# Optimization experiments

Hardware: AMD Instinct MI355X
Metric: run time of the kernel (lower is better)

## Reference

```python
import jax, jax.numpy as jnp
import numpy as np
import math

B, S, D, H = 2, 2048, 1024, 16
DH = D // H  # dim_per_head = 64


def setup_inputs() -> dict:
    key = jax.random.key(0)
    ks = jax.random.split(key, 12)
    s = 1.0 / math.sqrt(D)
    return {
        "key": jax.random.normal(ks[0], (B, S, D), jnp.float32),
        "value": jax.random.normal(ks[1], (B, S, D), jnp.float32),
        "query": jax.random.normal(ks[2], (B, S, D), jnp.float32),
        "mask": jax.random.randint(ks[3], (B, S, S), 0, 2).astype(bool),
        "Wq": jax.random.normal(ks[4], (D, D), jnp.float32) * s,
        "bq": jnp.zeros((D,), jnp.float32),
        "Wk": jax.random.normal(ks[5], (D, D), jnp.float32) * s,
        "bk": jnp.zeros((D,), jnp.float32),
        "Wv": jax.random.normal(ks[6], (D, D), jnp.float32) * s,
        "bv": jnp.zeros((D,), jnp.float32),
        "Wo": jax.random.normal(ks[7], (D, D), jnp.float32) * s,
        "bo": jnp.zeros((D,), jnp.float32),
    }


def _shape(x):
    # [B, S, D] -> [B, H, S, DH]
    return x.reshape(B, -1, H, DH).transpose(0, 2, 1, 3)


def reference(key, value, query, mask, Wq, bq, Wk, bk, Wv, bv, Wo, bo):
    q = _shape(query @ Wq.T + bq)  # [B,H,Sq,DH]
    k = _shape(key @ Wk.T + bk)    # [B,H,Sk,DH]
    v = _shape(value @ Wv.T + bv)  # [B,H,Sk,DH]
    q = q / jnp.sqrt(jnp.asarray(DH, q.dtype))
    scores = jnp.einsum("bhqd,bhkd->bhqk", q, k)
    scores = jnp.where(mask[:, None, :, :], jnp.asarray(-1e18, scores.dtype), scores)
    attn = jax.nn.softmax(scores, axis=-1)
    # dropout is identity in eval/deterministic reference
    ctx = jnp.einsum("bhqk,bhkd->bhqd", attn, v)
    ctx = ctx.transpose(0, 2, 1, 3).reshape(B, -1, D)  # unshape
    return ctx @ Wo.T + bo
```

## Files before the change

### kernel.cpp

```cpp
#include <hip/hip_runtime.h>
#include <math.h>


constexpr int Bc  = 2;
constexpr int Sc  = 2048;
constexpr int Dc  = 1024;
constexpr int Hc  = 16;
constexpr int DHc = 64;
constexpr int BSc = Bc * Sc;

constexpr float LOG2E = 1.4426950408889634f;

typedef __bf16 bf16x8 __attribute__((ext_vector_type(8)));
typedef __bf16 bf16x4 __attribute__((ext_vector_type(4)));
typedef float  f32x4  __attribute__((ext_vector_type(4)));

#define GLDS16(gp, lp) __builtin_amdgcn_global_load_lds( \
    (const __attribute__((address_space(1))) void*)(gp), \
    (__attribute__((address_space(3))) void*)(lp), 16, 0, 0)

__global__ __launch_bounds__(256)
void wsplit(const float* __restrict__ W0, const float* __restrict__ W1,
            const float* __restrict__ W2, const float* __restrict__ W3,
            __bf16* __restrict__ out)
{
    const float* src[4] = {W0, W1, W2, W3};
    const int z = blockIdx.y;
    const size_t idx = ((size_t)blockIdx.x * 256 + threadIdx.x) * 4;
    const float4 v = *(const float4*)&src[z][idx];
    bf16x4 o;
    o[0] = (__bf16)v.x; o[1] = (__bf16)v.y; o[2] = (__bf16)v.z; o[3] = (__bf16)v.w;
    *(bf16x4*)&out[(size_t)z * Dc * Dc + idx] = o;
}

__device__ __forceinline__ void sweep128s(const float* __restrict__ A,
                                          const __bf16* __restrict__ Wh,
                                          __bf16* As, __bf16* Ws,
                                          int gm0, int gn0, f32x4 acc[4][4])
{
    const int tid  = threadIdx.x;
    const int w    = tid >> 6;
    const int lane = tid & 63;
    const int cc   = lane & 15;
    const int g    = lane >> 4;
    const int wm   = (w & 1) * 64;
    const int wn   = (w >> 1) * 64;

    for (int k0 = 0; k0 < Dc; k0 += 64) {
        __syncthreads();
#pragma unroll
        for (int r = 0; r < 4; ++r) {
            const int L  = r * 256 + tid;
            const int wr = L >> 3;
            const int sl = L & 7;
            const int c  = sl ^ (wr & 7);
            GLDS16(Wh + (size_t)(gn0 + wr) * Dc + k0 + c * 8,
                   (char*)Ws + (r * 256 + w * 64) * 16);
        }
#pragma unroll
        for (int i = 0; i < 8; ++i) {
            const int Lq = i * 256 + tid;
            const int ar = Lq >> 4;
            const int aq = Lq & 15;
            const float4 v = *(const float4*)&A[(size_t)(gm0 + ar) * Dc + k0 + aq * 4];
            const int off = ar * 128 +
                        ((((aq >> 1) ^ (ar & 7)) << 4) | ((aq & 1) << 3));
            bf16x4 hv;
            hv[0] = (__bf16)v.x; hv[1] = (__bf16)v.y;
            hv[2] = (__bf16)v.z; hv[3] = (__bf16)v.w;
            *(bf16x4*)((char*)As + off) = hv;
        }
        __syncthreads();
#pragma unroll
        for (int kk = 0; kk < 2; ++kk) {
            const int cb4 = (kk * 4 + g) << 4;
            bf16x8 af[4], bfr[4];
#pragma unroll
            for (int mt = 0; mt < 4; ++mt) {
                const int row = wm + mt * 16 + cc;
                af[mt] = *(const bf16x8*)((const char*)As + row * 128 +
                                          (cb4 ^ ((row & 7) << 4)));
            }
#pragma unroll
            for (int nt = 0; nt < 4; ++nt) {
                const int row = wn + nt * 16 + cc;
                bfr[nt] = *(const bf16x8*)((const char*)Ws + row * 128 +
                                           (cb4 ^ ((row & 7) << 4)));
            }
#pragma unroll
            for (int mt = 0; mt < 4; ++mt)
#pragma unroll
                for (int nt = 0; nt < 4; ++nt)
                    acc[mt][nt] = __builtin_amdgcn_mfma_f32_16x16x32_bf16(
                        af[mt], bfr[nt], acc[mt][nt], 0, 0, 0);
        }
    }
}

__device__ __forceinline__ void sweep64b(const __bf16* __restrict__ Ahi,
                                         const __bf16* __restrict__ Alo,
                                         const __bf16* __restrict__ Wh,
                                         __bf16* AsHi, __bf16* AsLo, __bf16* Ws,
                                         int gm0, int gn0, f32x4 acc[2][4])
{
    const int tid  = threadIdx.x;
    const int w    = tid >> 6;
    const int lane = tid & 63;
    const int cc   = lane & 15;
    const int g    = lane >> 4;
    const int wm   = (w & 1) * 32;
    const int wn   = (w >> 1) * 64;

    for (int k0 = 0; k0 < Dc; k0 += 64) {
        __syncthreads();
#pragma unroll
        for (int r = 0; r < 4; ++r) {
            const int L  = r * 256 + tid;
            const int wr = L >> 3;
            const int sl = L & 7;
            const int c  = sl ^ (wr & 7);
            GLDS16(Wh + (size_t)(gn0 + wr) * Dc + k0 + c * 8,
                   (char*)Ws + (r * 256 + w * 64) * 16);
        }
#pragma unroll
        for (int r = 0; r < 2; ++r) {
            const int L  = r * 256 + tid;
            const int wr = L >> 3;
            const int sl = L & 7;
            const int c  = sl ^ (wr & 7);
            GLDS16(Ahi + (size_t)(gm0 + wr) * Dc + k0 + c * 8,
                   (char*)AsHi + (r * 256 + w * 64) * 16);
            GLDS16(Alo + (size_t)(gm0 + wr) * Dc + k0 + c * 8,
                   (char*)AsLo + (r * 256 + w * 64) * 16);
        }
        __syncthreads();
#pragma unroll
        for (int kk = 0; kk < 2; ++kk) {
            const int cb4 = (kk * 4 + g) << 4;
            bf16x8 ahi[2], alo[2], bfr[4];
#pragma unroll
            for (int mt = 0; mt < 2; ++mt) {
                const int row = wm + mt * 16 + cc;
                const int off = row * 128 + (cb4 ^ ((row & 7) << 4));
                ahi[mt] = *(const bf16x8*)((const char*)AsHi + off);
                alo[mt] = *(const bf16x8*)((const char*)AsLo + off);
            }
#pragma unroll
            for (int nt = 0; nt < 4; ++nt) {
                const int row = wn + nt * 16 + cc;
                bfr[nt] = *(const bf16x8*)((const char*)Ws + row * 128 +
                                           (cb4 ^ ((row & 7) << 4)));
            }
#pragma unroll
            for (int mt = 0; mt < 2; ++mt)
#pragma unroll
                for (int nt = 0; nt < 4; ++nt) {
                    acc[mt][nt] = __builtin_amdgcn_mfma_f32_16x16x32_bf16(
                        ahi[mt], bfr[nt], acc[mt][nt], 0, 0, 0);
                    acc[mt][nt] = __builtin_amdgcn_mfma_f32_16x16x32_bf16(
                        alo[mt], bfr[nt], acc[mt][nt], 0, 0, 0);
                }
        }
    }
}

__global__ __launch_bounds__(256)
void qkv_mfma(const float* __restrict__ query, const float* __restrict__ key,
              const float* __restrict__ value, const __bf16* __restrict__ Whi,
              const float* __restrict__ bq, const float* __restrict__ bk,
              const float* __restrict__ bv,
              __bf16* __restrict__ Qo, __bf16* __restrict__ Ko, __bf16* __restrict__ Vt)
{
    __shared__ __align__(16) __bf16 As[8192];
    __shared__ __align__(16) __bf16 Ws[8192];

    const int z = blockIdx.z;
    const float* A    = (z == 0) ? query : (z == 1) ? key : value;
    const float* bias = (z == 0) ? bq    : (z == 1) ? bk  : bv;
    const float scale = (z == 0) ? 0.125f * LOG2E : 1.0f;
    const __bf16* Wh  = Whi + (size_t)z * Dc * Dc;

    const int gm0 = blockIdx.x * 128;
    const int gn0 = blockIdx.y * 128;

    f32x4 acc[4][4];
#pragma unroll
    for (int mt = 0; mt < 4; ++mt)
#pragma unroll
        for (int nt = 0; nt < 4; ++nt) acc[mt][nt] = {0.f, 0.f, 0.f, 0.f};

    sweep128s(A, Wh, As, Ws, gm0, gn0, acc);

    const int tid = threadIdx.x;
    const int w = tid >> 6, lane = tid & 63;
    const int cc = lane & 15, g = lane >> 4;
    const int wm = (w & 1) * 64, wn = (w >> 1) * 64;

    float bias4[4];
#pragma unroll
    for (int nt = 0; nt < 4; ++nt) bias4[nt] = bias[gn0 + wn + nt * 16 + cc];

    if (z == 2) {
#pragma unroll
        for (int mt = 0; mt < 4; ++mt)
#pragma unroll
            for (int nt = 0; nt < 4; ++nt) {
                const int col = gn0 + wn + nt * 16 + cc;
                const int h = col >> 6, dh = col & 63;
                const int row0 = gm0 + wm + mt * 16 + g * 4;
                const int b = row0 >> 11, s0 = row0 & 2047;
                bf16x4 vv;
#pragma unroll
                for (int reg = 0; reg < 4; ++reg)
                    vv[reg] = (__bf16)(acc[mt][nt][reg] + bias4[nt]);
                *(bf16x4*)&Vt[(((size_t)(b * Hc + h)) * DHc + dh) * Sc + s0] = vv;
            }
    } else {
        __bf16* O = (z == 0) ? Qo : Ko;
#pragma unroll
        for (int mt = 0; mt < 4; ++mt)
#pragma unroll
            for (int nt = 0; nt < 4; ++nt) {
                const int col = gn0 + wn + nt * 16 + cc;
                const int h = col >> 6, dh = col & 63;
#pragma unroll
                for (int reg = 0; reg < 4; ++reg) {
                    const int row = gm0 + wm + mt * 16 + g * 4 + reg;
                    const int b = row >> 11, s = row & 2047;
                    O[(((size_t)(b * Hc + h)) * Sc + s) * DHc + dh] =
                        (__bf16)((acc[mt][nt][reg] + bias4[nt]) * scale);
                }
            }
    }
}

__global__ __launch_bounds__(256)
void out_mfma(const __bf16* __restrict__ ctxHi, const __bf16* __restrict__ ctxLo,
              const __bf16* __restrict__ Wohi,
              const float* __restrict__ bo, float* __restrict__ out)
{
    __shared__ __align__(16) __bf16 AsHi[4096];
    __shared__ __align__(16) __bf16 AsLo[4096];
    __shared__ __align__(16) __bf16 Ws[8192];

    const int gm0 = blockIdx.x * 64;
    const int gn0 = blockIdx.y * 128;

    f32x4 acc[2][4];
#pragma unroll
    for (int mt = 0; mt < 2; ++mt)
#pragma unroll
        for (int nt = 0; nt < 4; ++nt) acc[mt][nt] = {0.f, 0.f, 0.f, 0.f};

    sweep64b(ctxHi, ctxLo, Wohi, AsHi, AsLo, Ws, gm0, gn0, acc);

    const int tid = threadIdx.x;
    const int w = tid >> 6, lane = tid & 63;
    const int cc = lane & 15, g = lane >> 4;
    const int wm = (w & 1) * 32, wn = (w >> 1) * 64;

    float bias4[4];
#pragma unroll
    for (int nt = 0; nt < 4; ++nt) bias4[nt] = bo[gn0 + wn + nt * 16 + cc];

#pragma unroll
    for (int mt = 0; mt < 2; ++mt)
#pragma unroll
        for (int nt = 0; nt < 4; ++nt) {
            const int col = gn0 + wn + nt * 16 + cc;
#pragma unroll
            for (int reg = 0; reg < 4; ++reg) {
                const int row = gm0 + wm + mt * 16 + g * 4 + reg;
                out[(size_t)row * Dc + col] = acc[mt][nt][reg] + bias4[nt];
            }
        }
}

__global__ __launch_bounds__(256)
void mask_pack(const int* __restrict__ mask, unsigned long long* __restrict__ out)
{
    const int lane = threadIdx.x & 63;
    const size_t waveBase = ((size_t)blockIdx.x * 4 + (threadIdx.x >> 6)) * 256;
    unsigned long long b0 = __ballot(mask[waveBase + lane]        != 0);
    unsigned long long b1 = __ballot(mask[waveBase + 64 + lane]   != 0);
    unsigned long long b2 = __ballot(mask[waveBase + 128 + lane]  != 0);
    unsigned long long b3 = __ballot(mask[waveBase + 192 + lane]  != 0);
    if (lane == 0) {
        unsigned long long* dst = out + (waveBase >> 6);
        dst[0] = b0; dst[1] = b1; dst[2] = b2; dst[3] = b3;
    }
}

__global__ __launch_bounds__(512, 6)
void attn_mfma(const __bf16* __restrict__ Q, const __bf16* __restrict__ K,
               const __bf16* __restrict__ Vt,
               const unsigned long long* __restrict__ mp,
               __bf16* __restrict__ ctxHi, __bf16* __restrict__ ctxLo)
{
    __shared__ __align__(16) char smem[53248];

    const int tid  = threadIdx.x;
    const int w    = tid >> 6;
    const int lane = tid & 63;
    const int cc   = lane & 15;
    const int g    = lane >> 4;
    const int qg   = w & 3;
    const int kh   = w >> 2;
    const int bh   = blockIdx.y;
    const int b    = bh >> 4;
    const int h    = bh & 15;
    const int qw   = blockIdx.x * 64 + qg * 16;

    const __bf16* Qb  = Q  + (size_t)bh * Sc * DHc;
    const __bf16* Kb  = K  + (size_t)bh * Sc * DHc;
    const __bf16* Vtb = Vt + (size_t)bh * DHc * Sc;

    __bf16* Ks = (__bf16*)(smem + kh * 18432);
    __bf16* Vs = (__bf16*)(smem + kh * 18432 + 9216);
    char*   Pw = smem + 36864 + w * 2048;

    const bf16x8 qa0 = *(const bf16x8*)&Qb[(size_t)(qw + cc) * DHc + g * 8];
    const bf16x8 qa1 = *(const bf16x8*)&Qb[(size_t)(qw + cc) * DHc + 32 + g * 8];

    f32x4 o[4] = {};
    float l[4] = {0.f, 0.f, 0.f, 0.f};

    const int t4    = tid & 255;
    const int str_r = t4 >> 3;
    const int str_c = (t4 & 7) * 8;
    const int kbase = kh * (Sc / 2);

    bf16x8 pk0 = *(const bf16x8*)&Kb[(size_t)(kbase + str_r) * DHc + str_c];
    bf16x8 pk1 = *(const bf16x8*)&Kb[(size_t)(kbase + str_r + 32) * DHc + str_c];
    bf16x8 pv0 = *(const bf16x8*)&Vtb[(size_t)str_r * Sc + kbase + str_c];
    bf16x8 pv1 = *(const bf16x8*)&Vtb[(size_t)(str_r + 32) * Sc + kbase + str_c];

    for (int it = 0; it < 16; ++it) {
        const int k0 = kbase + it * 64;
        __syncthreads();
        *(bf16x8*)&Ks[(size_t)str_r * 72 + str_c]        = pk0;
        *(bf16x8*)&Ks[(size_t)(str_r + 32) * 72 + str_c] = pk1;
        *(bf16x8*)&Vs[(size_t)str_r * 72 + str_c]        = pv0;
        *(bf16x8*)&Vs[(size_t)(str_r + 32) * 72 + str_c] = pv1;
        __syncthreads();

        if (it < 15) {
            const int kn = k0 + 64;
            pk0 = *(const bf16x8*)&Kb[(size_t)(kn + str_r) * DHc + str_c];
            pk1 = *(const bf16x8*)&Kb[(size_t)(kn + str_r + 32) * DHc + str_c];
            pv0 = *(const bf16x8*)&Vtb[(size_t)str_r * Sc + kn + str_c];
            pv1 = *(const bf16x8*)&Vtb[(size_t)(str_r + 32) * Sc + kn + str_c];
        }

        unsigned long long mw[4];
#pragma unroll
        for (int r = 0; r < 4; ++r)
            mw[r] = mp[(size_t)(b * Sc + qw + g * 4 + r) * (Sc / 64) + (k0 >> 6)];

        f32x4 sc[4];
#pragma unroll
        for (int nt = 0; nt < 4; ++nt) {
            const bf16x8 kb0 = *(const bf16x8*)&Ks[(size_t)(nt * 16 + cc) * 72 + g * 8];
            const bf16x8 kb1 = *(const bf16x8*)&Ks[(size_t)(nt * 16 + cc) * 72 + 32 + g * 8];
            f32x4 z = {-24.f, -24.f, -24.f, -24.f};
            z = __builtin_amdgcn_mfma_f32_16x16x32_bf16(qa0, kb0, z, 0, 0, 0);
            z = __builtin_amdgcn_mfma_f32_16x16x32_bf16(qa1, kb1, z, 0, 0, 0);
            sc[nt] = z;
        }

        unsigned mlo[4], mhi[4];
#pragma unroll
        for (int r = 0; r < 4; ++r) {
            const unsigned long long sh = mw[r] >> cc;
            mlo[r] = (unsigned)sh;
            mhi[r] = (unsigned)(sh >> 32);
        }
#pragma unroll
        for (int nt = 0; nt < 4; ++nt)
#pragma unroll
            for (int r = 0; r < 4; ++r) {
                float p = __builtin_amdgcn_exp2f(sc[nt][r]);
                const unsigned bit =
                    (nt == 0) ? (mlo[r] & 1u) :
                    (nt == 1) ? (mlo[r] & 0x10000u) :
                    (nt == 2) ? (mhi[r] & 1u) : (mhi[r] & 0x10000u);
                p = bit ? 0.f : p;
                l[r] += p;
                *(__bf16*)(Pw + (g * 4 + r) * 128 + (((nt ^ g) << 5) | (cc << 1))) =
                    (__bf16)p;
            }

        const int sw = (cc >> 2) << 5;
        const bf16x8 pa0 = *(const bf16x8*)(Pw + cc * 128 + ((g * 16) ^ sw));
        const bf16x8 pa1 = *(const bf16x8*)(Pw + cc * 128 + ((64 + g * 16) ^ sw));

#pragma unroll
        for (int nt = 0; nt < 4; ++nt) {
            const bf16x8 vb0 = *(const bf16x8*)&Vs[(size_t)(nt * 16 + cc) * 72 + g * 8];
            const bf16x8 vb1 = *(const bf16x8*)&Vs[(size_t)(nt * 16 + cc) * 72 + 32 + g * 8];
            o[nt] = __builtin_amdgcn_mfma_f32_16x16x32_bf16(pa0, vb0, o[nt], 0, 0, 0);
            o[nt] = __builtin_amdgcn_mfma_f32_16x16x32_bf16(pa1, vb1, o[nt], 0, 0, 0);
        }
    }

#pragma unroll
    for (int off = 1; off < 16; off <<= 1)
#pragma unroll
        for (int r = 0; r < 4; ++r)
            l[r] += __shfl_xor(l[r], off, 16);

    __syncthreads();
    float* Oc = (float*)smem;
    float* Lc = (float*)(smem + 16384);
    if (kh) {
#pragma unroll
        for (int nt = 0; nt < 4; ++nt)
#pragma unroll
            for (int r = 0; r < 4; ++r)
                Oc[(qg * 16 + g * 4 + r) * 64 + nt * 16 + cc] = o[nt][r];
        if (cc == 0)
#pragma unroll
            for (int r = 0; r < 4; ++r) Lc[qg * 16 + g * 4 + r] = l[r];
    }
    __syncthreads();
    if (!kh) {
#pragma unroll
        for (int r = 0; r < 4; ++r) {
            const float lt = l[r] + Lc[qg * 16 + g * 4 + r];
            const float inv = 1.0f / lt;
            const int q = qw + g * 4 + r;
#pragma unroll
            for (int nt = 0; nt < 4; ++nt) {
                const size_t idx = ((size_t)b * Sc + q) * Dc + h * 64 + nt * 16 + cc;
                const float v =
                    (o[nt][r] + Oc[(qg * 16 + g * 4 + r) * 64 + nt * 16 + cc]) * inv;
                const __bf16 hi = (__bf16)v;
                ctxHi[idx] = hi;
                ctxLo[idx] = (__bf16)(v - (float)hi);
            }
        }
    }
}

extern "C" void kernel_launch(void* const* d_in, const int* in_sizes, int n_in,
                              void* d_out, int out_size, void* d_ws, size_t ws_size,
                              hipStream_t stream)
{
    const float* key   = (const float*)d_in[0];
    const float* value = (const float*)d_in[1];
    const float* query = (const float*)d_in[2];
    const int*   mask  = (const int*)  d_in[3];
    const float* Wq    = (const float*)d_in[4];
    const float* bq    = (const float*)d_in[5];
    const float* Wk    = (const float*)d_in[6];
    const float* bk    = (const float*)d_in[7];
    const float* Wv    = (const float*)d_in[8];
    const float* bv    = (const float*)d_in[9];
    const float* Wo    = (const float*)d_in[10];
    const float* bo    = (const float*)d_in[11];
    float* out = (float*)d_out;

    char* wsb = (char*)d_ws;
    __bf16* Qbf  = (__bf16*)(wsb);
    __bf16* Kbf  = (__bf16*)(wsb + ((size_t)8  << 20));
    __bf16* Vt   = (__bf16*)(wsb + ((size_t)16 << 20));
    unsigned long long* mpk = (unsigned long long*)(wsb + ((size_t)32 << 20));
    __bf16* Whi  = (__bf16*)(wsb + ((size_t)33 << 20));
    __bf16* ctxHi = (__bf16*)(wsb + ((size_t)41 << 20));
    __bf16* ctxLo = (__bf16*)(wsb + ((size_t)49 << 20));

    dim3 gws(Dc * Dc / (256 * 4), 4);
    wsplit<<<gws, 256, 0, stream>>>(Wq, Wk, Wv, Wo, Whi);

    dim3 gqkv(BSc / 128, Dc / 128, 3);
    qkv_mfma<<<gqkv, 256, 0, stream>>>(query, key, value, Whi, bq, bk, bv,
                                       Qbf, Kbf, Vt);

    const int mask_n = Bc * Sc * Sc;
    mask_pack<<<mask_n / 1024, 256, 0, stream>>>(mask, mpk);

    dim3 gattn(Sc / 64, Bc * Hc);
    attn_mfma<<<gattn, 512, 0, stream>>>(Qbf, Kbf, Vt, mpk, ctxHi, ctxLo);

    dim3 gout(BSc / 64, Dc / 128);
    out_mfma<<<gout, 256, 0, stream>>>(ctxHi, ctxLo, Whi + (size_t)3 * Dc * Dc,
                                       bo, out);
}
```

Baseline: 300.1 us.

## Double query rows per attention wave and XOR-swizzle K/V shared tiles

Each attention block now covers 128 queries instead of 64, with every wave handling two 16-row query tiles. This reuses each K/V fragment loaded from shared memory for twice the MFMA work and halves the number of K/V tile loads across the grid. The padded 72-element LDS rows are replaced by unpadded 128-byte rows with an XOR swizzle to avoid bank conflicts while saving shared memory. In exchange, register pressure rises (occupancy hint lowered from 6 to 4) and the grid has half as many blocks.

```diff
diff --git a/kernel.cpp b/kernel.cpp
--- a/kernel.cpp
+++ b/kernel.cpp
@@ -291,13 +291,13 @@
     }
 }
 
-__global__ __launch_bounds__(512, 6)
+__global__ __launch_bounds__(512, 4)
 void attn_mfma(const __bf16* __restrict__ Q, const __bf16* __restrict__ K,
                const __bf16* __restrict__ Vt,
                const unsigned long long* __restrict__ mp,
                __bf16* __restrict__ ctxHi, __bf16* __restrict__ ctxLo)
 {
-    __shared__ __align__(16) char smem[53248];
+    __shared__ __align__(16) char smem[49152];
 
     const int tid  = threadIdx.x;
     const int w    = tid >> 6;
@@ -309,136 +309,167 @@
     const int bh   = blockIdx.y;
     const int b    = bh >> 4;
     const int h    = bh & 15;
-    const int qw   = blockIdx.x * 64 + qg * 16;
+    const int qw   = blockIdx.x * 128 + qg * 32;
 
     const __bf16* Qb  = Q  + (size_t)bh * Sc * DHc;
     const __bf16* Kb  = K  + (size_t)bh * Sc * DHc;
     const __bf16* Vtb = Vt + (size_t)bh * DHc * Sc;
 
-    __bf16* Ks = (__bf16*)(smem + kh * 18432);
-    __bf16* Vs = (__bf16*)(smem + kh * 18432 + 9216);
-    char*   Pw = smem + 36864 + w * 2048;
-
-    const bf16x8 qa0 = *(const bf16x8*)&Qb[(size_t)(qw + cc) * DHc + g * 8];
-    const bf16x8 qa1 = *(const bf16x8*)&Qb[(size_t)(qw + cc) * DHc + 32 + g * 8];
-
-    f32x4 o[4] = {};
-    float l[4] = {0.f, 0.f, 0.f, 0.f};
-
-    const int t4    = tid & 255;
-    const int str_r = t4 >> 3;
-    const int str_c = (t4 & 7) * 8;
+    char* Ks = smem + kh * 16384;
+    char* Vs = smem + kh * 16384 + 8192;
+    char* Pw = smem + 32768 + w * 2048;
+
+    bf16x8 qa[2][2];
+#pragma unroll
+    for (int mt = 0; mt < 2; ++mt) {
+        qa[mt][0] = *(const bf16x8*)&Qb[(size_t)(qw + mt * 16 + cc) * DHc + g * 8];
+        qa[mt][1] = *(const bf16x8*)&Qb[(size_t)(qw + mt * 16 + cc) * DHc + 32 + g * 8];
+    }
+
+    f32x4 o[2][4] = {};
+    float l[2][4] = {};
+
+    const int t4 = tid & 255;
+    const int sr = t4 >> 3;
+    const int sl = t4 & 7;
+    const int ck = sl ^ (sr & 7);
     const int kbase = kh * (Sc / 2);
 
-    bf16x8 pk0 = *(const bf16x8*)&Kb[(size_t)(kbase + str_r) * DHc + str_c];
-    bf16x8 pk1 = *(const bf16x8*)&Kb[(size_t)(kbase + str_r + 32) * DHc + str_c];
-    bf16x8 pv0 = *(const bf16x8*)&Vtb[(size_t)str_r * Sc + kbase + str_c];
-    bf16x8 pv1 = *(const bf16x8*)&Vtb[(size_t)(str_r + 32) * Sc + kbase + str_c];
+    bf16x8 pk0 = *(const bf16x8*)&Kb[(size_t)(kbase + sr) * DHc + ck * 8];
+    bf16x8 pk1 = *(const bf16x8*)&Kb[(size_t)(kbase + sr + 32) * DHc + ck * 8];
+    bf16x8 pv0 = *(const bf16x8*)&Vtb[(size_t)sr * Sc + kbase + ck * 8];
+    bf16x8 pv1 = *(const bf16x8*)&Vtb[(size_t)(sr + 32) * Sc + kbase + ck * 8];
 
     for (int it = 0; it < 16; ++it) {
         const int k0 = kbase + it * 64;
         __syncthreads();
-        *(bf16x8*)&Ks[(size_t)str_r * 72 + str_c]        = pk0;
-        *(bf16x8*)&Ks[(size_t)(str_r + 32) * 72 + str_c] = pk1;
-        *(bf16x8*)&Vs[(size_t)str_r * 72 + str_c]        = pv0;
-        *(bf16x8*)&Vs[(size_t)(str_r + 32) * 72 + str_c] = pv1;
+        *(bf16x8*)(Ks + sr * 128 + sl * 16)        = pk0;
+        *(bf16x8*)(Ks + (sr + 32) * 128 + sl * 16) = pk1;
+        *(bf16x8*)(Vs + sr * 128 + sl * 16)        = pv0;
+        *(bf16x8*)(Vs + (sr + 32) * 128 + sl * 16) = pv1;
         __syncthreads();
 
         if (it < 15) {
             const int kn = k0 + 64;
-            pk0 = *(const bf16x8*)&Kb[(size_t)(kn + str_r) * DHc + str_c];
-            pk1 = *(const bf16x8*)&Kb[(size_t)(kn + str_r + 32) * DHc + str_c];
-            pv0 = *(const bf16x8*)&Vtb[(size_t)str_r * Sc + kn + str_c];
-            pv1 = *(const bf16x8*)&Vtb[(size_t)(str_r + 32) * Sc + kn + str_c];
-        }
-
-        unsigned long long mw[4];
-#pragma unroll
-        for (int r = 0; r < 4; ++r)
-            mw[r] = mp[(size_t)(b * Sc + qw + g * 4 + r) * (Sc / 64) + (k0 >> 6)];
-
-        f32x4 sc[4];
+            pk0 = *(const bf16x8*)&Kb[(size_t)(kn + sr) * DHc + ck * 8];
+            pk1 = *(const bf16x8*)&Kb[(size_t)(kn + sr + 32) * DHc + ck * 8];
+            pv0 = *(const bf16x8*)&Vtb[(size_t)sr * Sc + kn + ck * 8];
+            pv1 = *(const bf16x8*)&Vtb[(size_t)(sr + 32) * Sc + kn + ck * 8];
+        }
+
+        unsigned long long mw[2][4];
+#pragma unroll
+        for (int mt = 0; mt < 2; ++mt)
+#pragma unroll
+            for (int r = 0; r < 4; ++r)
+                mw[mt][r] = mp[(size_t)(b * Sc + qw + mt * 16 + g * 4 + r) * (Sc / 64)
+                               + (k0 >> 6)];
+
+        f32x4 sc[2][4];
 #pragma unroll
         for (int nt = 0; nt < 4; ++nt) {
-            const bf16x8 kb0 = *(const bf16x8*)&Ks[(size_t)(nt * 16 + cc) * 72 + g * 8];
-            const bf16x8 kb1 = *(const bf16x8*)&Ks[(size_t)(nt * 16 + cc) * 72 + 32 + g * 8];
-            f32x4 z = {-24.f, -24.f, -24.f, -24.f};
-            z = __builtin_amdgcn_mfma_f32_16x16x32_bf16(qa0, kb0, z, 0, 0, 0);
-            z = __builtin_amdgcn_mfma_f32_16x16x32_bf16(qa1, kb1, z, 0, 0, 0);
-            sc[nt] = z;
-        }
-
-        unsigned mlo[4], mhi[4];
-#pragma unroll
-        for (int r = 0; r < 4; ++r) {
-            const unsigned long long sh = mw[r] >> cc;
-            mlo[r] = (unsigned)sh;
-            mhi[r] = (unsigned)(sh >> 32);
-        }
-#pragma unroll
-        for (int nt = 0; nt < 4; ++nt)
+            const int row = nt * 16 + cc;
+            const int rx  = (row & 7) << 4;
+            const bf16x8 kb0 = *(const bf16x8*)(Ks + row * 128 + ((g << 4) ^ rx));
+            const bf16x8 kb1 = *(const bf16x8*)(Ks + row * 128 + ((64 + (g << 4)) ^ rx));
+            f32x4 z0 = {-24.f, -24.f, -24.f, -24.f};
+            z0 = __builtin_amdgcn_mfma_f32_16x16x32_bf16(qa[0][0], kb0, z0, 0, 0, 0);
+            z0 = __builtin_amdgcn_mfma_f32_16x16x32_bf16(qa[0][1], kb1, z0, 0, 0, 0);
+            sc[0][nt] = z0;
+            f32x4 z1 = {-24.f, -24.f, -24.f, -24.f};
+            z1 = __builtin_amdgcn_mfma_f32_16x16x32_bf16(qa[1][0], kb0, z1, 0, 0, 0);
+            z1 = __builtin_amdgcn_mfma_f32_16x16x32_bf16(qa[1][1], kb1, z1, 0, 0, 0);
+            sc[1][nt] = z1;
+        }
+
+        bf16x8 pa[2][2];
+#pragma unroll
+        for (int mt = 0; mt < 2; ++mt) {
+            unsigned mlo[4], mhi[4];
 #pragma unroll
             for (int r = 0; r < 4; ++r) {
-                float p = __builtin_amdgcn_exp2f(sc[nt][r]);
-                const unsigned bit =
-                    (nt == 0) ? (mlo[r] & 1u) :
-                    (nt == 1) ? (mlo[r] & 0x10000u) :
-                    (nt == 2) ? (mhi[r] & 1u) : (mhi[r] & 0x10000u);
-                p = bit ? 0.f : p;
-                l[r] += p;
-                *(__bf16*)(Pw + (g * 4 + r) * 128 + (((nt ^ g) << 5) | (cc << 1))) =
-                    (__bf16)p;
-            }
-
-        const int sw = (cc >> 2) << 5;
-        const bf16x8 pa0 = *(const bf16x8*)(Pw + cc * 128 + ((g * 16) ^ sw));
-        const bf16x8 pa1 = *(const bf16x8*)(Pw + cc * 128 + ((64 + g * 16) ^ sw));
+                const unsigned long long sh = mw[mt][r] >> cc;
+                mlo[r] = (unsigned)sh;
+                mhi[r] = (unsigned)(sh >> 32);
+            }
+#pragma unroll
+            for (int nt = 0; nt < 4; ++nt)
+#pragma unroll
+                for (int r = 0; r < 4; ++r) {
+                    float p = __builtin_amdgcn_exp2f(sc[mt][nt][r]);
+                    const unsigned bit =
+                        (nt == 0) ? (mlo[r] & 1u) :
+                        (nt == 1) ? (mlo[r] & 0x10000u) :
+                        (nt == 2) ? (mhi[r] & 1u) : (mhi[r] & 0x10000u);
+                    p = bit ? 0.f : p;
+                    l[mt][r] += p;
+                    *(__bf16*)(Pw + (g * 4 + r) * 128 +
+                               (((nt ^ g) << 5) | (cc << 1))) = (__bf16)p;
+                }
+            const int sw = (cc >> 2) << 5;
+            pa[mt][0] = *(const bf16x8*)(Pw + cc * 128 + ((g * 16) ^ sw));
+            pa[mt][1] = *(const bf16x8*)(Pw + cc * 128 + ((64 + g * 16) ^ sw));
+        }
 
 #pragma unroll
         for (int nt = 0; nt < 4; ++nt) {
-            const bf16x8 vb0 = *(const bf16x8*)&Vs[(size_t)(nt * 16 + cc) * 72 + g * 8];
-            const bf16x8 vb1 = *(const bf16x8*)&Vs[(size_t)(nt * 16 + cc) * 72 + 32 + g * 8];
-            o[nt] = __builtin_amdgcn_mfma_f32_16x16x32_bf16(pa0, vb0, o[nt], 0, 0, 0);
-            o[nt] = __builtin_amdgcn_mfma_f32_16x16x32_bf16(pa1, vb1, o[nt], 0, 0, 0);
+            const int row = nt * 16 + cc;
+            const int rx  = (row & 7) << 4;
+            const bf16x8 vb0 = *(const bf16x8*)(Vs + row * 128 + ((g << 4) ^ rx));
+            const bf16x8 vb1 = *(const bf16x8*)(Vs + row * 128 + ((64 + (g << 4)) ^ rx));
+            o[0][nt] = __builtin_amdgcn_mfma_f32_16x16x32_bf16(pa[0][0], vb0, o[0][nt], 0, 0, 0);
+            o[0][nt] = __builtin_amdgcn_mfma_f32_16x16x32_bf16(pa[0][1], vb1, o[0][nt], 0, 0, 0);
+            o[1][nt] = __builtin_amdgcn_mfma_f32_16x16x32_bf16(pa[1][0], vb0, o[1][nt], 0, 0, 0);
+            o[1][nt] = __builtin_amdgcn_mfma_f32_16x16x32_bf16(pa[1][1], vb1, o[1][nt], 0, 0, 0);
         }
     }
 
 #pragma unroll
     for (int off = 1; off < 16; off <<= 1)
 #pragma unroll
-        for (int r = 0; r < 4; ++r)
-            l[r] += __shfl_xor(l[r], off, 16);
+        for (int mt = 0; mt < 2; ++mt)
+#pragma unroll
+            for (int r = 0; r < 4; ++r)
+                l[mt][r] += __shfl_xor(l[mt][r], off, 16);
 
     __syncthreads();
-    float* Oc = (float*)smem;
-    float* Lc = (float*)(smem + 16384);
+    float* Oc = (float*)(smem + 16384);
+    float* Lc = (float*)smem;
     if (kh) {
 #pragma unroll
-        for (int nt = 0; nt < 4; ++nt)
-#pragma unroll
-            for (int r = 0; r < 4; ++r)
-                Oc[(qg * 16 + g * 4 + r) * 64 + nt * 16 + cc] = o[nt][r];
-        if (cc == 0)
-#pragma unroll
-            for (int r = 0; r < 4; ++r) Lc[qg * 16 + g * 4 + r] = l[r];
+        for (int mt = 0; mt < 2; ++mt) {
+#pragma unroll
+            for (int nt = 0; nt < 4; ++nt)
+#pragma unroll
+                for (int r = 0; r < 4; ++r)
+                    Oc[(qg * 32 + mt * 16 + g * 4 + r) * 64 + nt * 16 + cc] =
+                        o[mt][nt][r];
+            if (cc == 0)
+#pragma unroll
+                for (int r = 0; r < 4; ++r)
+                    Lc[qg * 32 + mt * 16 + g * 4 + r] = l[mt][r];
+        }
     }
     __syncthreads();
     if (!kh) {
 #pragma unroll
-        for (int r = 0; r < 4; ++r) {
-            const float lt = l[r] + Lc[qg * 16 + g * 4 + r];
-            const float inv = 1.0f / lt;
-            const int q = qw + g * 4 + r;
-#pragma unroll
-            for (int nt = 0; nt < 4; ++nt) {
-                const size_t idx = ((size_t)b * Sc + q) * Dc + h * 64 + nt * 16 + cc;
-                const float v =
-                    (o[nt][r] + Oc[(qg * 16 + g * 4 + r) * 64 + nt * 16 + cc]) * inv;
-                const __bf16 hi = (__bf16)v;
-                ctxHi[idx] = hi;
-                ctxLo[idx] = (__bf16)(v - (float)hi);
-            }
-        }
+        for (int mt = 0; mt < 2; ++mt)
+#pragma unroll
+            for (int r = 0; r < 4; ++r) {
+                const int row = qg * 32 + mt * 16 + g * 4 + r;
+                const float lt = l[mt][r] + Lc[row];
+                const float inv = 1.0f / lt;
+                const int q = blockIdx.x * 128 + row;
+#pragma unroll
+                for (int nt = 0; nt < 4; ++nt) {
+                    const size_t idx =
+                        ((size_t)b * Sc + q) * Dc + h * 64 + nt * 16 + cc;
+                    const float v = (o[mt][nt][r] + Oc[row * 64 + nt * 16 + cc]) * inv;
+                    const __bf16 hi = (__bf16)v;
+                    ctxHi[idx] = hi;
+                    ctxLo[idx] = (__bf16)(v - (float)hi);
+                }
+            }
     }
 }
 
@@ -479,7 +510,7 @@
     const int mask_n = Bc * Sc * Sc;
     mask_pack<<<mask_n / 1024, 256, 0, stream>>>(mask, mpk);
 
-    dim3 gattn(Sc / 64, Bc * Hc);
+    dim3 gattn(Sc / 128, Bc * Hc);
     attn_mfma<<<gattn, 512, 0, stream>>>(Qbf, Kbf, Vt, mpk, ctxHi, ctxLo);
 
     dim3 gout(BSc / 64, Dc / 128);
```

After: 374.0 us. 1.25x slower.
